# Kernel optimization log

Hardware: AMD Instinct MI355X
Metric: run time of the kernel (lower is better)

Reference implementation:

```python
import jax, jax.numpy as jnp
import numpy as np

IN_FEATURES = 4096
OUT_FEATURES = 4096
BLOCK_SIZE = 64
LOWRANK_DIM = 64
BATCH = 4096  # flat batch of tokens


def _butterfly_forward_indices(out_features, in_features, block_size):
    """Replicates lean_transformer.get_butterfly_indices forward_indices for the
    square case where butterfly_size == num_blocks (here 4096/64 = 64).
    Block (p, q) is active iff p ^ q has popcount <= 1 (identity + all log2(n) butterfly factors).
    """
    nob = out_features // block_size  # num output blocks
    nib = in_features // block_size   # num input blocks
    p = np.arange(nob)[:, None]
    q = np.arange(nib)[None, :]
    x = p ^ q
    layout = (x & (x - 1)) == 0  # True when x == 0 or x is a power of two
    a_out = int(layout.sum(1)[0])  # active input blocks per output block
    a_in = int(layout.sum(0)[0])   # active output blocks per input block
    input_block_index = np.nonzero(layout)[1].reshape(nob, a_out)
    output_block_index = np.nonzero(layout.T)[1].reshape(nib, a_in)
    # for output block p and its s-th active input block j, find which of j's
    # active output slots points back to p
    gathered = output_block_index[input_block_index]  # [nob, a_out, a_in]
    active = np.argmax(gathered == np.arange(nob)[:, None, None], axis=-1)
    return (input_block_index * a_in + active).astype(np.int32)


def setup_inputs() -> dict:
    key = jax.random.key(0)
    k1, k2, k3, k4 = jax.random.split(key, 4)
    std = float(np.sqrt(2.0 / (5 * min(OUT_FEATURES, IN_FEATURES))))
    fwd_idx = _butterfly_forward_indices(OUT_FEATURES, IN_FEATURES, BLOCK_SIZE)
    a_in = fwd_idx.size // (IN_FEATURES // BLOCK_SIZE)  # active blocks per input
    return {
        "input": jax.random.normal(k1, (BATCH, IN_FEATURES), jnp.float32),
        "weight": jax.random.normal(k2, (IN_FEATURES, a_in, BLOCK_SIZE), jnp.float32) * std,
        "lowrank_first": jax.random.normal(k3, (LOWRANK_DIM, IN_FEATURES), jnp.float32) * std,
        "lowrank_second": jax.random.normal(k4, (OUT_FEATURES, LOWRANK_DIM), jnp.float32) * std,
        "forward_indices": jnp.asarray(fwd_idx),  # [num_output_blocks, a_out] int32
    }


def _butterfly_matmul(x, weight, forward_indices):
    # x: [B, in_features]; weight: [in_features, a_in, block_size]
    batch = x.shape[0]
    in_f, a_in, bs = weight.shape
    nib = in_f // bs
    xb = x.reshape(batch, nib, bs)                     # [B, nib, bs]
    w = weight.reshape(nib, bs, a_in, bs)              # [nib, bs, a_in, bs]
    # per-input-block contributions to each of its a_in candidate output blocks
    contrib = jnp.einsum("bjk,jkac->bjac", xb, w)      # [B, nib, a_in, bs]
    contrib = contrib.reshape(batch, nib * a_in, bs)
    # gather the contributions feeding each output block and accumulate
    out = contrib[:, forward_indices, :].sum(axis=2)   # [B, nob, bs]
    return out.reshape(batch, -1)                      # [B, out_features]


def reference(input, weight, lowrank_first, lowrank_second, forward_indices):
    out = _butterfly_matmul(input, weight, forward_indices)
    # low-rank correction: F.linear(F.linear(x, W1), W2, out)
    out = out + (input @ lowrank_first.T) @ lowrank_second.T
    return out
```

## Files before the change

### kernel.cpp

```cpp
#include <hip/hip_runtime.h>
#include <hip/hip_bf16.h>


#define DEVINL __device__ __forceinline__

typedef __attribute__((ext_vector_type(8))) short bfx8;
typedef __attribute__((ext_vector_type(4))) float fx4;

DEVINL short f2bf(float f) {
  unsigned u = __builtin_bit_cast(unsigned, f);
  unsigned r = 0x7FFFu + ((u >> 16) & 1u);
  return (short)((u + r) >> 16);
}

DEVINL int swzb(int row, int kbyte) { return (row << 7) + (kbyte ^ ((row & 7) << 4)); }

DEVINL void gload16(const void* g, void* l) {
  __builtin_amdgcn_global_load_lds(
      (const __attribute__((address_space(1))) unsigned int*)g,
      (__attribute__((address_space(3))) unsigned int*)l, 16, 0, 0);
}

__global__ __launch_bounds__(256) void prep_all_kern(
    const float* __restrict__ weight, const float* __restrict__ w1,
    const float* __restrict__ w2, const int* __restrict__ fwd,
    const float* __restrict__ x, unsigned short* __restrict__ bmat,
    unsigned short* __restrict__ w1b, unsigned short* __restrict__ xb) {
  int cid = blockIdx.x, tid = threadIdx.x;
  if (cid >= 576) {
    int gid = (cid - 576) * 256 + tid;
    int b = gid >> 9, c8 = gid & 511;
    int j = c8 >> 3, c0 = (c8 & 7) << 3;
    const float* src = x + (size_t)b * 4096 + j * 64 + c0;
    fx4 v0 = *(const fx4*)src;
    fx4 v1 = *(const fx4*)(src + 4);
    bfx8 o;
    o[0] = f2bf(v0[0]); o[1] = f2bf(v0[1]); o[2] = f2bf(v0[2]); o[3] = f2bf(v0[3]);
    o[4] = f2bf(v1[0]); o[5] = f2bf(v1[1]); o[6] = f2bf(v1[2]); o[7] = f2bf(v1[3]);
    size_t off = (size_t)j * 262144 + (size_t)b * 64 + ((((c0 << 1) ^ ((b & 7) << 4))) >> 1);
    *(bfx8*)(xb + off) = o;
    return;
  }
  if (cid < 512) {
    int p = cid >> 3, t = cid & 7;
    unsigned short* dst = bmat + (size_t)cid * 4096;
    if (t < 7) {
      int idx = fwd[p * 7 + t];
      int j = idx / 7, a = idx - j * 7;
      int k = tid >> 2, n0 = (tid & 3) << 4;
      const float* src = weight + ((size_t)(j * 64 + k) * 7 + a) * 64 + n0;
#pragma unroll
      for (int e = 0; e < 16; ++e) {
        int n = n0 + e;
        dst[(n << 6) + ((((k << 1) ^ ((n & 7) << 4))) >> 1)] = f2bf(src[e]);
      }
    } else {
      int n = tid >> 2, r0 = (tid & 3) << 4;
      const float* src = w2 + ((size_t)(p * 64 + n)) * 64 + r0;
#pragma unroll
      for (int e = 0; e < 16; ++e) {
        int k = r0 + e;
        dst[(n << 6) + ((((k << 1) ^ ((n & 7) << 4))) >> 1)] = f2bf(src[e]);
      }
    }
  } else {
    int jc = cid - 512;
    unsigned short* dst = w1b + (size_t)jc * 4096;
    int r = tid >> 2, k0 = (tid & 3) << 4;
    const float* src = w1 + (size_t)r * 4096 + jc * 64 + k0;
#pragma unroll
    for (int e = 0; e < 16; ++e) {
      int k = k0 + e;
      dst[(r << 6) + ((((k << 1) ^ ((r & 7) << 4))) >> 1)] = f2bf(src[e]);
    }
  }
}

__global__ __launch_bounds__(256) void compute_t_split(const unsigned short* __restrict__ xb,
                                                       const unsigned short* __restrict__ w1b,
                                                       float* __restrict__ part) {
  __shared__ char smem[32768];
  int rt = blockIdx.x >> 3, kc = blockIdx.x & 7;
  int tid = threadIdx.x, lane = tid & 63, w = tid >> 6;
  int lr = lane & 15, lkb = (lane >> 4) << 4;

  auto stage = [&](int jc, int buf) {
    const unsigned short* sa = xb + (size_t)(kc * 8 + jc) * 262144 + (size_t)rt * 4096;
    const unsigned short* sb = w1b + (size_t)(kc * 8 + jc) * 4096;
    char* da = smem + buf * 8192;
    char* db = smem + 16384 + buf * 8192;
#pragma unroll
    for (int i = 0; i < 2; ++i) {
      gload16(sa + tid * 8 + i * 2048, da + tid * 16 + i * 4096);
      gload16(sb + tid * 8 + i * 2048, db + tid * 16 + i * 4096);
    }
  };

  fx4 acc[4] = {};
  stage(0, 0);
#pragma unroll 1
  for (int jc = 0; jc < 8; ++jc) {
    __syncthreads();
    int cur = jc & 1;
    if (jc < 7) stage(jc + 1, cur ^ 1);
    const char* ab = smem + cur * 8192;
    const char* bb = smem + 16384 + cur * 8192;
#pragma unroll
    for (int kk = 0; kk < 2; ++kk) {
      bfx8 af = *(const bfx8*)(ab + swzb(w * 16 + lr, kk * 64 + lkb));
#pragma unroll
      for (int ni = 0; ni < 4; ++ni) {
        bfx8 bf = *(const bfx8*)(bb + swzb(ni * 16 + lr, kk * 64 + lkb));
        acc[ni] = __builtin_amdgcn_mfma_f32_16x16x32_bf16(af, bf, acc[ni], 0, 0, 0);
      }
    }
  }
  float* pb = part + (size_t)kc * 262144 + (size_t)rt * 4096;
#pragma unroll
  for (int ni = 0; ni < 4; ++ni)
#pragma unroll
    for (int r = 0; r < 4; ++r) {
      int row = w * 16 + (lane >> 4) * 4 + r;
      pb[(size_t)row * 64 + ni * 16 + lr] = acc[ni][r];
    }
}

__global__ __launch_bounds__(256) void reduce_t_kern(const float* __restrict__ part,
                                                     unsigned short* __restrict__ tb) {
  int gid = blockIdx.x * 256 + threadIdx.x;
  int b = gid >> 3, c0 = (gid & 7) << 3;
  const float* pp = part + (size_t)b * 64 + c0;
  fx4 s0 = {0.f, 0.f, 0.f, 0.f}, s1 = {0.f, 0.f, 0.f, 0.f};
#pragma unroll
  for (int kc = 0; kc < 8; ++kc) {
    s0 += *(const fx4*)(pp + (size_t)kc * 262144);
    s1 += *(const fx4*)(pp + (size_t)kc * 262144 + 4);
  }
  bfx8 o;
#pragma unroll
  for (int e = 0; e < 4; ++e) { o[e] = f2bf(s0[e]); o[e + 4] = f2bf(s1[e]); }
  *(bfx8*)(tb + (size_t)b * 64 + ((((c0 << 1) ^ ((b & 7) << 4))) >> 1)) = o;
}

__global__ __launch_bounds__(512, 6) void butterfly_main(
    const unsigned short* __restrict__ xb, const unsigned short* __restrict__ tb,
    const unsigned short* __restrict__ bmat, const int* __restrict__ fwd,
    float* __restrict__ out) {
  __shared__ char smem[49152];
  int bid = blockIdx.x;
  int wid = (bid & 7) * 256 + (bid >> 3);
  int mt = wid >> 6, p = wid & 63;
  int tid = threadIdx.x, lane = tid & 63, w = tid >> 6;
  int lr = lane & 15, lkb = (lane >> 4) << 4;

  auto stageA = [&](int c, int buf) {
    const unsigned short* src;
    if (c < 7) {
      int j = fwd[p * 7 + c] / 7;
      src = xb + ((size_t)j * 4096 + mt * 128) * 64;
    } else {
      src = tb + (size_t)(mt * 128) * 64;
    }
    char* dst = smem + buf * 16384;
    gload16(src + tid * 8, dst + tid * 16);
    gload16(src + tid * 8 + 4096, dst + tid * 16 + 8192);
  };
  auto stageB = [&](int t, int buf) {
    const unsigned short* src = bmat + ((size_t)(p * 8 + t)) * 4096;
    gload16(src + tid * 8, smem + 32768 + buf * 8192 + tid * 16);
  };

  fx4 acc[4] = {};
  stageA(0, 0);
  stageB(0, 0);
#pragma unroll 1
  for (int t = 0; t < 8; ++t) {
    __syncthreads();
    int cur = t & 1;
    if (t < 7) { stageA(t + 1, cur ^ 1); stageB(t + 1, cur ^ 1); }
    const char* ab = smem + cur * 16384;
    const char* bb = smem + 32768 + cur * 8192;
#pragma unroll
    for (int kk = 0; kk < 2; ++kk) {
      bfx8 af = *(const bfx8*)(ab + swzb(w * 16 + lr, kk * 64 + lkb));
#pragma unroll
      for (int ni = 0; ni < 4; ++ni) {
        bfx8 bf = *(const bfx8*)(bb + swzb(ni * 16 + lr, kk * 64 + lkb));
        acc[ni] = __builtin_amdgcn_mfma_f32_16x16x32_bf16(af, bf, acc[ni], 0, 0, 0);
      }
    }
  }

  size_t rbase = (size_t)(mt * 128 + w * 16) * 4096 + p * 64;
#pragma unroll
  for (int ni = 0; ni < 4; ++ni)
#pragma unroll
    for (int r = 0; r < 4; ++r)
      out[rbase + (size_t)((lane >> 4) * 4 + r) * 4096 + ni * 16 + lr] = acc[ni][r];
}

__global__ void naive_t_kern(const float* __restrict__ x, const float* __restrict__ w1,
                             float* __restrict__ t) {
  int gid = blockIdx.x * 256 + threadIdx.x;
  int b = gid >> 6, r = gid & 63;
  const float* xr = x + (size_t)b * 4096;
  const float* wr = w1 + (size_t)r * 4096;
  float s = 0.f;
  for (int k = 0; k < 4096; ++k) s += xr[k] * wr[k];
  t[gid] = s;
}

__global__ void naive_out_kern(const float* __restrict__ x, const float* __restrict__ weight,
                               const float* __restrict__ w2, const int* __restrict__ fwd,
                               const float* __restrict__ t, float* __restrict__ out) {
  size_t gid = (size_t)blockIdx.x * 256 + threadIdx.x;
  int b = (int)(gid >> 12), o = (int)(gid & 4095);
  int p = o >> 6, n = o & 63;
  float s = 0.f;
  for (int si = 0; si < 7; ++si) {
    int idx = fwd[p * 7 + si], j = idx / 7, a = idx - j * 7;
    const float* xr = x + (size_t)b * 4096 + j * 64;
    for (int k = 0; k < 64; ++k)
      s += xr[k] * weight[((size_t)(j * 64 + k) * 7 + a) * 64 + n];
  }
  const float* tr = t + (size_t)b * 64;
  const float* w2r = w2 + (size_t)o * 64;
  for (int r = 0; r < 64; ++r) s += tr[r] * w2r[r];
  out[gid] = s;
}

extern "C" void kernel_launch(void* const* d_in, const int* in_sizes, int n_in,
                              void* d_out, int out_size, void* d_ws, size_t ws_size,
                              hipStream_t stream) {
  const float* x = (const float*)d_in[0];
  const float* weight = (const float*)d_in[1];
  const float* w1 = (const float*)d_in[2];
  const float* w2 = (const float*)d_in[3];
  const int* fwd = (const int*)d_in[4];
  float* out = (float*)d_out;

  const size_t XB_E = 16777216;
  const size_t TB_E = 262144;
  const size_t BM_E = 2097152;
  const size_t W1_E = 262144;
  const size_t BASE_B = (XB_E + TB_E + BM_E + W1_E) * 2;

  if (ws_size >= BASE_B) {
    unsigned short* xb = (unsigned short*)d_ws;
    unsigned short* tb = xb + XB_E;
    unsigned short* bmat = tb + TB_E;
    unsigned short* w1b = bmat + BM_E;
    float* part = out;
    prep_all_kern<<<8768, 256, 0, stream>>>(weight, w1, w2, fwd, x, bmat, w1b, xb);
    compute_t_split<<<512, 256, 0, stream>>>(xb, w1b, part);
    reduce_t_kern<<<128, 256, 0, stream>>>(part, tb);
    butterfly_main<<<2048, 512, 0, stream>>>(xb, tb, bmat, fwd, out);
  } else {
    float* t = (float*)d_ws;
    naive_t_kern<<<1024, 256, 0, stream>>>(x, w1, t);
    naive_out_kern<<<65536, 256, 0, stream>>>(x, weight, w2, fwd, t, out);
  }
}
```

Measured before the change: 75.24 us.

## Retile butterfly GEMM to 64-row tiles spanning four output blocks per workgroup

The main butterfly kernel now uses 256-thread workgroups that each handle 64 batch rows and four consecutive output blocks, in a 32-step pipelined loop, instead of 128 rows and one output block. Each workgroup writes a contiguous 256-column output strip, and the grid halves to 1024 workgroups with less LDS per workgroup. The goal is better write coalescing and more independent accumulators per wave. In exchange, input tiles are staged separately for each of the four output blocks, so reuse of the A tiles drops and register pressure rises from sixteen accumulators.

```diff
diff --git a/kernel.cpp b/kernel.cpp
--- a/kernel.cpp
+++ b/kernel.cpp
@@ -142,61 +142,68 @@
   *(bfx8*)(tb + (size_t)b * 64 + ((((c0 << 1) ^ ((b & 7) << 4))) >> 1)) = o;
 }
 
-__global__ __launch_bounds__(512, 6) void butterfly_main(
+__global__ __launch_bounds__(256, 4) void butterfly_mp(
     const unsigned short* __restrict__ xb, const unsigned short* __restrict__ tb,
     const unsigned short* __restrict__ bmat, const int* __restrict__ fwd,
     float* __restrict__ out) {
-  __shared__ char smem[49152];
+  __shared__ char smem[32768];
   int bid = blockIdx.x;
-  int wid = (bid & 7) * 256 + (bid >> 3);
-  int mt = wid >> 6, p = wid & 63;
+  int wid = (bid & 7) * 128 + (bid >> 3);
+  int mt = wid >> 4, pg = wid & 15;
   int tid = threadIdx.x, lane = tid & 63, w = tid >> 6;
   int lr = lane & 15, lkb = (lane >> 4) << 4;
 
-  auto stageA = [&](int c, int buf) {
-    const unsigned short* src;
-    if (c < 7) {
-      int j = fwd[p * 7 + c] / 7;
-      src = xb + ((size_t)j * 4096 + mt * 128) * 64;
+  auto stage = [&](int s, int buf) {
+    int qq = s >> 3, tt = s & 7;
+    int ps = pg * 4 + qq;
+    const unsigned short* srcA;
+    if (tt < 7) {
+      int j = fwd[ps * 7 + tt] / 7;
+      srcA = xb + ((size_t)j * 4096 + mt * 64) * 64;
     } else {
-      src = tb + (size_t)(mt * 128) * 64;
-    }
-    char* dst = smem + buf * 16384;
-    gload16(src + tid * 8, dst + tid * 16);
-    gload16(src + tid * 8 + 4096, dst + tid * 16 + 8192);
+      srcA = tb + (size_t)(mt * 64) * 64;
+    }
+    char* da = smem + buf * 8192;
+    gload16(srcA + tid * 8, da + tid * 16);
+    gload16(srcA + tid * 8 + 2048, da + tid * 16 + 4096);
+    const unsigned short* srcB = bmat + ((size_t)(ps * 8 + tt)) * 4096;
+    char* db = smem + 16384 + buf * 8192;
+    gload16(srcB + tid * 8, db + tid * 16);
+    gload16(srcB + tid * 8 + 2048, db + tid * 16 + 4096);
   };
-  auto stageB = [&](int t, int buf) {
-    const unsigned short* src = bmat + ((size_t)(p * 8 + t)) * 4096;
-    gload16(src + tid * 8, smem + 32768 + buf * 8192 + tid * 16);
-  };
-
-  fx4 acc[4] = {};
-  stageA(0, 0);
-  stageB(0, 0);
+
+  fx4 acc[4][4] = {};
+  stage(0, 0);
+#pragma unroll
+  for (int q = 0; q < 4; ++q) {
 #pragma unroll 1
-  for (int t = 0; t < 8; ++t) {
-    __syncthreads();
-    int cur = t & 1;
-    if (t < 7) { stageA(t + 1, cur ^ 1); stageB(t + 1, cur ^ 1); }
-    const char* ab = smem + cur * 16384;
-    const char* bb = smem + 32768 + cur * 8192;
-#pragma unroll
-    for (int kk = 0; kk < 2; ++kk) {
-      bfx8 af = *(const bfx8*)(ab + swzb(w * 16 + lr, kk * 64 + lkb));
-#pragma unroll
-      for (int ni = 0; ni < 4; ++ni) {
-        bfx8 bf = *(const bfx8*)(bb + swzb(ni * 16 + lr, kk * 64 + lkb));
-        acc[ni] = __builtin_amdgcn_mfma_f32_16x16x32_bf16(af, bf, acc[ni], 0, 0, 0);
-      }
-    }
-  }
-
-  size_t rbase = (size_t)(mt * 128 + w * 16) * 4096 + p * 64;
-#pragma unroll
-  for (int ni = 0; ni < 4; ++ni)
-#pragma unroll
-    for (int r = 0; r < 4; ++r)
-      out[rbase + (size_t)((lane >> 4) * 4 + r) * 4096 + ni * 16 + lr] = acc[ni][r];
+    for (int t = 0; t < 8; ++t) {
+      int s = q * 8 + t;
+      __syncthreads();
+      if (s < 31) stage(s + 1, (s + 1) & 1);
+      const char* ab = smem + (s & 1) * 8192;
+      const char* bb = smem + 16384 + (s & 1) * 8192;
+#pragma unroll
+      for (int kk = 0; kk < 2; ++kk) {
+        bfx8 af = *(const bfx8*)(ab + swzb(w * 16 + lr, kk * 64 + lkb));
+#pragma unroll
+        for (int ni = 0; ni < 4; ++ni) {
+          bfx8 bf = *(const bfx8*)(bb + swzb(ni * 16 + lr, kk * 64 + lkb));
+          acc[q][ni] = __builtin_amdgcn_mfma_f32_16x16x32_bf16(af, bf, acc[q][ni], 0, 0, 0);
+        }
+      }
+    }
+  }
+
+  size_t rbase = (size_t)(mt * 64 + w * 16) * 4096 + pg * 256;
+#pragma unroll
+  for (int q = 0; q < 4; ++q)
+#pragma unroll
+    for (int ni = 0; ni < 4; ++ni)
+#pragma unroll
+      for (int r = 0; r < 4; ++r)
+        out[rbase + (size_t)((lane >> 4) * 4 + r) * 4096 + q * 64 + ni * 16 + lr] =
+            acc[q][ni][r];
 }
 
 __global__ void naive_t_kern(const float* __restrict__ x, const float* __restrict__ w1,
@@ -254,7 +261,7 @@
     prep_all_kern<<<8768, 256, 0, stream>>>(weight, w1, w2, fwd, x, bmat, w1b, xb);
     compute_t_split<<<512, 256, 0, stream>>>(xb, w1b, part);
     reduce_t_kern<<<128, 256, 0, stream>>>(part, tb);
-    butterfly_main<<<2048, 512, 0, stream>>>(xb, tb, bmat, fwd, out);
+    butterfly_mp<<<1024, 256, 0, stream>>>(xb, tb, bmat, fwd, out);
   } else {
     float* t = (float*)d_ws;
     naive_t_kern<<<1024, 256, 0, stream>>>(x, w1, t);
```

Result: faster. 68.67 us (-8.7%).
